# Kernel tuning notes

Hardware: AMD Instinct MI355X
Metric: run time of the kernel (lower is better)

The kernel has to match this reference:

```python
import jax, jax.numpy as jnp
import numpy as np

NEG_SLOPE = 0.01  # torch F.leaky_relu default


def _gcn(x, W, b, src, dst, w, n_nodes):
    # PyG GCNConv(normalize=False, add_self_loops=False):
    # out[i] = sum_{e:(j->i)} w_e * (x @ W)[j] + b
    xw = x @ W                              # [N, out]
    msg = w[:, None] * xw[src]              # [E, out] gather
    return jax.ops.segment_sum(msg, dst, num_segments=n_nodes) + b


def setup_inputs() -> dict:
    key = jax.random.key(0)
    ks = jax.random.split(key, 12)
    N, E, B = 50000, 800000, 50
    d_in, d_hid, d_out = 128, 128, 128
    nodes_per_graph = N // B

    features = jax.random.normal(ks[0], (N, d_in), dtype=jnp.float32)
    adjs = jax.random.randint(ks[1], (2, E), 0, N, dtype=jnp.int32)
    values = jax.random.uniform(ks[2], (E,), dtype=jnp.float32)
    # root of graph g is its first node
    root_idx = jnp.arange(B, dtype=jnp.int32) * nodes_per_graph
    knowledge_node_num = jnp.full((B,), nodes_per_graph, dtype=jnp.int32)
    knowledge_edge_num = jnp.full((B,), E // B, dtype=jnp.int32)
    batch = jnp.arange(N, dtype=jnp.int32) // nodes_per_graph

    scale = 1.0 / np.sqrt(d_in)
    W1 = jax.random.uniform(ks[3], (d_in, d_hid), jnp.float32, -scale, scale)
    b1 = jax.random.uniform(ks[4], (d_hid,), jnp.float32, -scale, scale)
    W2 = jax.random.uniform(ks[5], (d_hid + d_in, d_out), jnp.float32, -scale, scale)
    b2 = jax.random.uniform(ks[6], (d_out,), jnp.float32, -scale, scale)
    Wl = jax.random.uniform(ks[7], (d_out + d_hid, d_in), jnp.float32, -scale, scale)
    bl = jax.random.uniform(ks[8], (d_in,), jnp.float32, -scale, scale)

    return {"features": features, "values": values, "W1": W1, "b1": b1,
            "W2": W2, "b2": b2, "Wl": Wl, "bl": bl,
            "adjs": adjs, "root_idx": root_idx,
            "knowledge_node_num": knowledge_node_num,
            "knowledge_edge_num": knowledge_edge_num, "batch": batch}


def reference(features, values, W1, b1, W2, b2, Wl, bl,
              adjs, root_idx, knowledge_node_num, knowledge_edge_num, batch):
    N = features.shape[0]
    B = knowledge_node_num.shape[0]
    src, dst = adjs[0], adjs[1]

    # per-node graph id (replaces the python loop building batch_k)
    batch_k = jnp.repeat(jnp.arange(B), knowledge_node_num, total_repeat_length=N)

    x0 = features                                    # features_1
    h1 = _gcn(x0, W1, b1, src, dst, values, N)       # conv1; features_2

    # root_extend: each node gets the raw features of its graph's root
    root1 = x0[root_idx[batch_k]]                    # [N, d_in]
    h = jax.nn.leaky_relu(jnp.concatenate([h1, root1], axis=1), NEG_SLOPE)
    # dropout=0.0 -> identity

    h2 = jax.nn.leaky_relu(_gcn(h, W2, b2, src, dst, values, N), NEG_SLOPE)

    root2 = h1[root_idx[batch_k]]                    # [N, d_hid] from conv1 output
    h = jnp.concatenate([h2, root2], axis=1)
    out = jax.nn.leaky_relu(h @ Wl + bl, NEG_SLOPE)
    return out
```

## Files before the change

### kernel.cpp

```cpp
#include <hip/hip_runtime.h>
#include <hip/hip_bf16.h>

#define NEG_SLOPE 0.01f
#define NBUK_MAX 256
#define ATILE 2048

typedef __attribute__((ext_vector_type(8))) short short8;
typedef __attribute__((ext_vector_type(4))) float f32x4;

__device__ __forceinline__ float lrelu(float x) { return x > 0.f ? x : NEG_SLOPE * x; }

__device__ __forceinline__ unsigned short f2bf(float f) {
    unsigned u = __builtin_bit_cast(unsigned, f);
    u += 0x7fffu + ((u >> 16) & 1u);
    return (unsigned short)(u >> 16);
}
__device__ __forceinline__ float bf2f(unsigned short h) {
    return __builtin_bit_cast(float, (unsigned)h << 16);
}
__device__ __forceinline__ float bflo(unsigned u) {
    return __builtin_bit_cast(float, u << 16);
}
__device__ __forceinline__ float bfhi(unsigned u) {
    return __builtin_bit_cast(float, u & 0xffff0000u);
}

__global__ __launch_bounds__(256) void prep_kernel(
        const float* __restrict__ features, const int* __restrict__ batch,
        const int* __restrict__ root_idx, const float* __restrict__ W1,
        const float* __restrict__ W2, const float* __restrict__ Wl,
        unsigned short* __restrict__ feat16, int* __restrict__ rmap,
        int* __restrict__ bucket_count, unsigned short* __restrict__ wt1,
        unsigned short* __restrict__ wt2, unsigned short* __restrict__ wtl,
        int N, int nbuk) {
    const int total = N * 32;
    for (int i = blockIdx.x * blockDim.x + threadIdx.x; i < total;
         i += gridDim.x * blockDim.x) {
        float4 v = *(const float4*)(features + (size_t)i * 4);
        ushort4 p;
        p.x = f2bf(v.x); p.y = f2bf(v.y); p.z = f2bf(v.z); p.w = f2bf(v.w);
        *(ushort4*)(feat16 + (size_t)i * 4) = p;
        if (i < N) rmap[i] = root_idx[batch[i]];
        if (i < nbuk) bucket_count[i] = 0;
        if (i < 128 * 128) {
            int k = i >> 7, c = i & 127;
            wt1[c * 128 + k] = f2bf(W1[i]);
        }
        if (i < 256 * 128) {
            int k = i >> 7, c = i & 127;
            wt2[c * 256 + k] = f2bf(W2[i]);
            wtl[c * 256 + k] = f2bf(Wl[i]);
        }
    }
}

__global__ __launch_bounds__(256) void histA_kernel(const int* __restrict__ dst,
                                                    int* __restrict__ bucket_count,
                                                    int E, int nbuk) {
    __shared__ int hist[NBUK_MAX];
    if (threadIdx.x < nbuk) hist[threadIdx.x] = 0;
    __syncthreads();
    for (int e = blockIdx.x * blockDim.x + threadIdx.x; e < E; e += gridDim.x * blockDim.x)
        atomicAdd(&hist[dst[e] >> 8], 1);
    __syncthreads();
    if (threadIdx.x < nbuk) {
        int v = hist[threadIdx.x];
        if (v) atomicAdd(&bucket_count[threadIdx.x], v);
    }
}

__global__ __launch_bounds__(256) void scanA_kernel(const int* __restrict__ bucket_count,
                                                    int* __restrict__ bucket_base,
                                                    int* __restrict__ bucket_cursor,
                                                    int* __restrict__ rowstart,
                                                    int N, int E, int nbuk) {
    __shared__ int sb[256];
    const int t = threadIdx.x;
    int v = (t < nbuk) ? bucket_count[t] : 0;
    sb[t] = v;
    __syncthreads();
    for (int off = 1; off < 256; off <<= 1) {
        int x = (t >= off) ? sb[t - off] : 0;
        __syncthreads();
        sb[t] += x;
        __syncthreads();
    }
    if (t < nbuk) {
        int ex = sb[t] - v;
        bucket_base[t] = ex;
        bucket_cursor[t] = ex;
    }
    if (t == 0) {
        bucket_base[nbuk] = sb[255];
        rowstart[N] = E;
    }
}

__global__ __launch_bounds__(256) void binA_kernel(const int* __restrict__ src,
                                                   const int* __restrict__ dst,
                                                   const float* __restrict__ vals,
                                                   int* __restrict__ bucket_cursor,
                                                   int2* __restrict__ bstage,
                                                   int E, int nbuk) {
    __shared__ int hist[NBUK_MAX];
    __shared__ int lbase[NBUK_MAX + 1];
    __shared__ int gbase[NBUK_MAX];
    __shared__ int cur[NBUK_MAX];
    __shared__ int scanbuf[256];
    __shared__ int2 stage[ATILE];
    const int tid = threadIdx.x;
    const int t0 = blockIdx.x * ATILE;
    const int cnt = min(ATILE, E - t0);

    if (tid < nbuk) hist[tid] = 0;
    __syncthreads();

    int s8[8], d8[8], v8[8];
#pragma unroll
    for (int k = 0; k < 8; ++k) {
        const int li = k * 256 + tid;
        const bool ok = li < cnt;
        const int idx = t0 + li;
        s8[k] = ok ? src[idx] : 0;
        d8[k] = ok ? dst[idx] : 0;
        v8[k] = ok ? ((const int*)vals)[idx] : 0;
        if (ok) atomicAdd(&hist[d8[k] >> 8], 1);
    }
    __syncthreads();
    const int h = (tid < nbuk) ? hist[tid] : 0;
    scanbuf[tid] = h;
    __syncthreads();
    for (int off = 1; off < 256; off <<= 1) {
        int x = (tid >= off) ? scanbuf[tid - off] : 0;
        __syncthreads();
        scanbuf[tid] += x;
        __syncthreads();
    }
    if (tid < nbuk) {
        const int ex = scanbuf[tid] - h;
        lbase[tid] = ex;
        cur[tid] = ex;
        gbase[tid] = h ? atomicAdd(&bucket_cursor[tid], h) : 0;
    }
    if (tid == 0) lbase[nbuk] = cnt;
    __syncthreads();
#pragma unroll
    for (int k = 0; k < 8; ++k) {
        if ((k * 256 + tid) < cnt) {
            const int b = d8[k] >> 8;
            const int lp = atomicAdd(&cur[b], 1);
            stage[lp] = make_int2((s8[k] & 0xffff) | ((d8[k] & 255) << 16), v8[k]);
        }
    }
    __syncthreads();
    for (int i = tid; i < cnt; i += 256) {
        int lo = 0, hi = nbuk;
        while (hi - lo > 1) {
            const int mid = (lo + hi) >> 1;
            if (lbase[mid] <= i) lo = mid; else hi = mid;
        }
        bstage[gbase[lo] + (i - lbase[lo])] = stage[i];
    }
}

__global__ __launch_bounds__(256) void binB_kernel(const int2* __restrict__ bstage,
                                                   const int* __restrict__ bucket_base,
                                                   int* __restrict__ rowstart,
                                                   int2* __restrict__ edata, int N) {
    __shared__ int deg_l[256];
    __shared__ int pfx[256];
    const int b = blockIdx.x;
    const int base = bucket_base[b], end = bucket_base[b + 1];
    const int n0 = b << 8;
    const int tid = threadIdx.x;
    deg_l[tid] = 0;
    __syncthreads();
    for (int i = base + tid; i < end; i += 256)
        atomicAdd(&deg_l[(bstage[i].x >> 16) & 255], 1);
    __syncthreads();
    const int v = deg_l[tid];
    pfx[tid] = v;
    __syncthreads();
    for (int off = 1; off < 256; off <<= 1) {
        int x = (tid >= off) ? pfx[tid - off] : 0;
        __syncthreads();
        pfx[tid] += x;
        __syncthreads();
    }
    const int ex = pfx[tid] - v;
    if (n0 + tid < N) rowstart[n0 + tid] = base + ex;
    __syncthreads();
    deg_l[tid] = ex;
    __syncthreads();
    for (int i = base + tid; i < end; i += 256) {
        const int2 r = bstage[i];
        const int lp = atomicAdd(&deg_l[(r.x >> 16) & 255], 1);
        edata[base + lp] = make_int2(r.x & 0xffff, r.y);
    }
}

__global__ __launch_bounds__(256) void gather_kernel(const unsigned short* __restrict__ xw,
                                                     const int* __restrict__ rowstart,
                                                     const int2* __restrict__ edata,
                                                     const float* __restrict__ bias,
                                                     unsigned short* __restrict__ h, int N) {
    const int node = blockIdx.x * 4 + (threadIdx.x >> 6);
    const int lane = threadIdx.x & 63;
    if (node >= N) return;
    const int s0 = rowstart[node], s1 = rowstart[node + 1];
    float2 acc = *(const float2*)(bias + lane * 2);
    int e = s0;
    for (; e + 4 <= s1; e += 4) {
        int2 e0 = edata[e], e1 = edata[e + 1], e2 = edata[e + 2], e3 = edata[e + 3];
        unsigned xa = *(const unsigned*)(xw + (size_t)e0.x * 128 + lane * 2);
        unsigned xb = *(const unsigned*)(xw + (size_t)e1.x * 128 + lane * 2);
        unsigned xc = *(const unsigned*)(xw + (size_t)e2.x * 128 + lane * 2);
        unsigned xd = *(const unsigned*)(xw + (size_t)e3.x * 128 + lane * 2);
        float va = __builtin_bit_cast(float, e0.y), vb = __builtin_bit_cast(float, e1.y);
        float vc = __builtin_bit_cast(float, e2.y), vd = __builtin_bit_cast(float, e3.y);
        acc.x = fmaf(va, bflo(xa), acc.x);
        acc.y = fmaf(va, bfhi(xa), acc.y);
        acc.x = fmaf(vb, bflo(xb), acc.x);
        acc.y = fmaf(vb, bfhi(xb), acc.y);
        acc.x = fmaf(vc, bflo(xc), acc.x);
        acc.y = fmaf(vc, bfhi(xc), acc.y);
        acc.x = fmaf(vd, bflo(xd), acc.x);
        acc.y = fmaf(vd, bfhi(xd), acc.y);
    }
    for (; e < s1; ++e) {
        int2 e0 = edata[e];
        float va = __builtin_bit_cast(float, e0.y);
        unsigned xa = *(const unsigned*)(xw + (size_t)e0.x * 128 + lane * 2);
        acc.x = fmaf(va, bflo(xa), acc.x);
        acc.y = fmaf(va, bfhi(xa), acc.y);
    }
    unsigned pk = (unsigned)f2bf(acc.x) | ((unsigned)f2bf(acc.y) << 16);
    *(unsigned*)(h + (size_t)node * 128 + lane * 2) = pk;
}

template <int K, bool LRA, bool LRB, bool LROUT, bool HASB, bool OUTBF>
__global__ __launch_bounds__(256) void mgemm_kernel(const unsigned short* __restrict__ A,
                                                    const unsigned short* __restrict__ B2,
                                                    const int* __restrict__ rmap,
                                                    const unsigned short* __restrict__ Wt,
                                                    const float* __restrict__ bias,
                                                    void* __restrict__ outv, int N) {
    __shared__ short As[64 * 32];
    __shared__ short Bs[128 * 32];
    const int tid = threadIdx.x;
    const int wv = tid >> 6, lane = tid & 63;
    const int lr = lane & 15, lg = lane >> 4;
    const int row0 = blockIdx.x * 64;

    const int arow = tid >> 2, apart = tid & 3;
    const int grow = row0 + arow;
    const int gr = grow < N ? grow : N - 1;
    const int rr = (K > 128) ? rmap[gr] : 0;
    const int bc = tid & 127, bhalf = (tid >> 7) * 16;

    f32x4 acc[8];
#pragma unroll
    for (int t = 0; t < 8; ++t) acc[t] = (f32x4){0.f, 0.f, 0.f, 0.f};

#pragma unroll 1
    for (int kc = 0; kc < K / 32; ++kc) {
        const int k0 = kc * 32;
        {
            const int kbase = k0 + apart * 8;
            const bool inA = kbase < 128;
            const unsigned short* sp = inA ? A + (size_t)gr * 128 + kbase
                                           : B2 + (size_t)rr * 128 + (kbase - 128);
            short8 v = *(const short8*)sp;
            const bool dolr = inA ? LRA : LRB;
            if (dolr) {
#pragma unroll
                for (int j = 0; j < 8; ++j)
                    v[j] = (short)f2bf(lrelu(bf2f((unsigned short)v[j])));
            }
            *(short8*)&As[arow * 32 + apart * 8] = v;
        }
        {
            const unsigned short* wsrc = Wt + (size_t)bc * K + k0 + bhalf;
            *(short8*)&Bs[bc * 32 + bhalf]     = *(const short8*)wsrc;
            *(short8*)&Bs[bc * 32 + bhalf + 8] = *(const short8*)(wsrc + 8);
        }
        __syncthreads();
        short8 af = *(short8*)&As[(wv * 16 + lr) * 32 + lg * 8];
#pragma unroll
        for (int t = 0; t < 8; ++t) {
            short8 bf = *(short8*)&Bs[(t * 16 + lr) * 32 + lg * 8];
            acc[t] = __builtin_amdgcn_mfma_f32_16x16x32_bf16(af, bf, acc[t], 0, 0, 0);
        }
        __syncthreads();
    }

#pragma unroll
    for (int t = 0; t < 8; ++t) {
#pragma unroll
        for (int r = 0; r < 4; ++r) {
            int grr = row0 + wv * 16 + lg * 4 + r;
            if (grr < N) {
                float v = acc[t][r];
                if (HASB) v += bias[t * 16 + lr];
                if (LROUT) v = lrelu(v);
                if (OUTBF)
                    ((unsigned short*)outv)[(size_t)grr * 128 + t * 16 + lr] = f2bf(v);
                else
                    ((float*)outv)[(size_t)grr * 128 + t * 16 + lr] = v;
            }
        }
    }
}

extern "C" void kernel_launch(void* const* d_in, const int* in_sizes, int n_in,
                              void* d_out, int out_size, void* d_ws, size_t ws_size,
                              hipStream_t stream) {
    const float* features = (const float*)d_in[0];
    const float* values   = (const float*)d_in[1];
    const float* W1 = (const float*)d_in[2];
    const float* b1 = (const float*)d_in[3];
    const float* W2 = (const float*)d_in[4];
    const float* b2 = (const float*)d_in[5];
    const float* Wl = (const float*)d_in[6];
    const float* bl = (const float*)d_in[7];
    const int* adjs     = (const int*)d_in[8];
    const int* root_idx = (const int*)d_in[9];
    const int* batch    = (const int*)d_in[12];
    float* out = (float*)d_out;

    const int N = in_sizes[0] / 128;
    const int E = in_sizes[1];
    const int* src = adjs;
    const int* dst = adjs + E;
    const int nbuk = (N + 255) >> 8;

    const size_t nf = (size_t)N * 128;
    unsigned short* bufA   = (unsigned short*)d_ws;
    unsigned short* h1     = bufA + nf;
    unsigned short* h2     = h1 + nf;
    unsigned short* feat16 = h2 + nf;
    unsigned short* wt1 = feat16 + nf;
    unsigned short* wt2 = wt1 + 128 * 128;
    unsigned short* wtl = wt2 + 256 * 128;
    uintptr_t ep = ((uintptr_t)(wtl + 256 * 128) + 7) & ~(uintptr_t)7;
    int2* edata  = (int2*)ep;
    int2* bstage = edata + E;
    int*  rmap     = (int*)(bstage + E);
    int*  rowstart = rmap + N;
    int*  bucket_count  = rowstart + N + 1;
    int*  bucket_base   = bucket_count + NBUK_MAX;
    int*  bucket_cursor = bucket_base + NBUK_MAX + 1;

    const int gblocks = (N + 63) / 64;

    prep_kernel<<<1024, 256, 0, stream>>>(features, batch, root_idx, W1, W2, Wl,
                                          feat16, rmap, bucket_count, wt1, wt2, wtl,
                                          N, nbuk);
    histA_kernel<<<256, 256, 0, stream>>>(dst, bucket_count, E, nbuk);
    scanA_kernel<<<1, 256, 0, stream>>>(bucket_count, bucket_base, bucket_cursor,
                                        rowstart, N, E, nbuk);
    binA_kernel<<<(E + ATILE - 1) / ATILE, 256, 0, stream>>>(src, dst, values,
                                                             bucket_cursor, bstage, E, nbuk);
    binB_kernel<<<nbuk, 256, 0, stream>>>(bstage, bucket_base, rowstart, edata, N);

    mgemm_kernel<128, false, false, false, false, true>
        <<<gblocks, 256, 0, stream>>>(feat16, nullptr, nullptr, wt1, nullptr, bufA, N);
    gather_kernel<<<(N + 3) / 4, 256, 0, stream>>>(bufA, rowstart, edata, b1, h1, N);

    mgemm_kernel<256, true, true, false, false, true>
        <<<gblocks, 256, 0, stream>>>(h1, feat16, rmap, wt2, nullptr, bufA, N);
    gather_kernel<<<(N + 3) / 4, 256, 0, stream>>>(bufA, rowstart, edata, b2, h2, N);

    mgemm_kernel<256, true, false, true, true, false>
        <<<gblocks, 256, 0, stream>>>(h2, h1, rmap, wtl, bl, out, N);
}
```

Measured before the change: 273.0 us.

## Preload full weight matrix into swizzled LDS and stream A fragments from registers

The GEMM kernel now loads the whole transposed weight (128xK) into XOR-swizzled shared memory once per block. Each lane then reads its A fragment directly from global memory into registers, prefetching the next k-chunk, which removes the per-iteration A staging through LDS and both barriers. Blocks grow to 512 threads covering 128 rows, halving the block count. In exchange it uses up to 64KB of LDS per block, which may limit occupancy, and the A loads are uncoalesced per-row 16-byte reads.

```diff
diff --git a/kernel.cpp b/kernel.cpp
--- a/kernel.cpp
+++ b/kernel.cpp
@@ -239,59 +239,68 @@
 }
 
 template <int K, bool LRA, bool LRB, bool LROUT, bool HASB, bool OUTBF>
-__global__ __launch_bounds__(256) void mgemm_kernel(const unsigned short* __restrict__ A,
+__global__ __launch_bounds__(512) void mgemm_kernel(const unsigned short* __restrict__ A,
                                                     const unsigned short* __restrict__ B2,
                                                     const int* __restrict__ rmap,
                                                     const unsigned short* __restrict__ Wt,
                                                     const float* __restrict__ bias,
                                                     void* __restrict__ outv, int N) {
-    __shared__ short As[64 * 32];
-    __shared__ short Bs[128 * 32];
+    __shared__ short Bs[128 * K];
     const int tid = threadIdx.x;
     const int wv = tid >> 6, lane = tid & 63;
     const int lr = lane & 15, lg = lane >> 4;
-    const int row0 = blockIdx.x * 64;
-
-    const int arow = tid >> 2, apart = tid & 3;
-    const int grow = row0 + arow;
-    const int gr = grow < N ? grow : N - 1;
+    const int row0 = blockIdx.x * 128;
+
+    {
+        const int col = tid >> 2, part = tid & 3;
+        const int swz = (col & 7) << 3;
+#pragma unroll
+        for (int i = 0; i < K / 32; ++i) {
+            const int k = part * (K / 4) + i * 8;
+            short8 v = *(const short8*)(Wt + (size_t)col * K + k);
+            *(short8*)&Bs[col * K + (k ^ swz)] = v;
+        }
+    }
+    __syncthreads();
+
+    const int row = row0 + wv * 16 + lr;
+    const int gr = row < N ? row : N - 1;
     const int rr = (K > 128) ? rmap[gr] : 0;
-    const int bc = tid & 127, bhalf = (tid >> 7) * 16;
+    const unsigned short* aptr = A + (size_t)gr * 128;
+    const unsigned short* bptr = (K > 128) ? B2 + (size_t)rr * 128 : nullptr;
 
     f32x4 acc[8];
 #pragma unroll
     for (int t = 0; t < 8; ++t) acc[t] = (f32x4){0.f, 0.f, 0.f, 0.f};
 
+    auto loadraw = [&](int kc) -> short8 {
+        const int kbase = kc * 32 + lg * 8;
+        if (K == 128 || kbase < 128) return *(const short8*)(aptr + kbase);
+        return *(const short8*)(bptr + (kbase - 128));
+    };
+    auto xform = [&](short8 v, int kc) -> short8 {
+        const bool dolr = (K == 128 || kc * 32 < 128) ? LRA : LRB;
+        if (dolr) {
+#pragma unroll
+            for (int j = 0; j < 8; ++j)
+                v[j] = (short)f2bf(lrelu(bf2f((unsigned short)v[j])));
+        }
+        return v;
+    };
+
+    short8 raw = loadraw(0);
 #pragma unroll 1
     for (int kc = 0; kc < K / 32; ++kc) {
-        const int k0 = kc * 32;
-        {
-            const int kbase = k0 + apart * 8;
-            const bool inA = kbase < 128;
-            const unsigned short* sp = inA ? A + (size_t)gr * 128 + kbase
-                                           : B2 + (size_t)rr * 128 + (kbase - 128);
-            short8 v = *(const short8*)sp;
-            const bool dolr = inA ? LRA : LRB;
-            if (dolr) {
-#pragma unroll
-                for (int j = 0; j < 8; ++j)
-                    v[j] = (short)f2bf(lrelu(bf2f((unsigned short)v[j])));
-            }
-            *(short8*)&As[arow * 32 + apart * 8] = v;
-        }
-        {
-            const unsigned short* wsrc = Wt + (size_t)bc * K + k0 + bhalf;
-            *(short8*)&Bs[bc * 32 + bhalf]     = *(const short8*)wsrc;
-            *(short8*)&Bs[bc * 32 + bhalf + 8] = *(const short8*)(wsrc + 8);
-        }
-        __syncthreads();
-        short8 af = *(short8*)&As[(wv * 16 + lr) * 32 + lg * 8];
+        short8 raw_nxt = (kc + 1 < K / 32) ? loadraw(kc + 1) : raw;
+        short8 af = xform(raw, kc);
+        const int kb = kc * 32 + lg * 8;
 #pragma unroll
         for (int t = 0; t < 8; ++t) {
-            short8 bf = *(short8*)&Bs[(t * 16 + lr) * 32 + lg * 8];
+            const int col = t * 16 + lr;
+            short8 bf = *(short8*)&Bs[col * K + (kb ^ ((col & 7) << 3))];
             acc[t] = __builtin_amdgcn_mfma_f32_16x16x32_bf16(af, bf, acc[t], 0, 0, 0);
         }
-        __syncthreads();
+        raw = raw_nxt;
     }
 
 #pragma unroll
@@ -351,7 +360,7 @@
     int*  bucket_base   = bucket_count + NBUK_MAX;
     int*  bucket_cursor = bucket_base + NBUK_MAX + 1;
 
-    const int gblocks = (N + 63) / 64;
+    const int gblocks = (N + 127) / 128;
 
     prep_kernel<<<1024, 256, 0, stream>>>(features, batch, root_idx, W1, W2, Wl,
                                           feat16, rmap, bucket_count, wt1, wt2, wtl,
@@ -364,13 +373,13 @@
     binB_kernel<<<nbuk, 256, 0, stream>>>(bstage, bucket_base, rowstart, edata, N);
 
     mgemm_kernel<128, false, false, false, false, true>
-        <<<gblocks, 256, 0, stream>>>(feat16, nullptr, nullptr, wt1, nullptr, bufA, N);
+        <<<gblocks, 512, 0, stream>>>(feat16, nullptr, nullptr, wt1, nullptr, bufA, N);
     gather_kernel<<<(N + 3) / 4, 256, 0, stream>>>(bufA, rowstart, edata, b1, h1, N);
 
     mgemm_kernel<256, true, true, false, false, true>
-        <<<gblocks, 256, 0, stream>>>(h1, feat16, rmap, wt2, nullptr, bufA, N);
+        <<<gblocks, 512, 0, stream>>>(h1, feat16, rmap, wt2, nullptr, bufA, N);
     gather_kernel<<<(N + 3) / 4, 256, 0, stream>>>(bufA, rowstart, edata, b2, h2, N);
 
     mgemm_kernel<256, true, false, true, true, false>
-        <<<gblocks, 256, 0, stream>>>(h2, h1, rmap, wtl, bl, out, N);
-}
+        <<<gblocks, 512, 0, stream>>>(h2, h1, rmap, wtl, bl, out, N);
+}
```

Measured after the change: 268.1 us. No clear change (-1.8%).
